# Optimization experiments

Hardware: AMD Instinct MI355X
Metric: run time of the kernel (lower is better)

## Reference

```python
import jax, jax.numpy as jnp
import numpy as np

B, C, H, W = 8, 256, 128, 128
RED = 4
LAMBDA_C = 0.5
LAMBDA_S = 0.5
EPS = 1e-5  # BatchNorm eps (eval mode: running stats)


def setup_inputs() -> dict:
    key = jax.random.key(0)
    ks = jax.random.split(key, 8)
    Cr = C // RED
    x1 = jax.random.normal(ks[0], (B, C, H, W), jnp.float32)
    x2 = jax.random.normal(ks[1], (B, C, H, W), jnp.float32)
    # feature_extractor: 1x1 conv (dim*2 -> dim), kaiming-ish scale
    w_fe = jax.random.normal(ks[2], (C, 2 * C), jnp.float32) * (2.0 / (2 * C)) ** 0.5
    bn_gamma = jnp.ones((C,), jnp.float32)
    bn_beta = jnp.zeros((C,), jnp.float32)
    bn_mean = jnp.zeros((C,), jnp.float32)
    bn_var = jnp.ones((C,), jnp.float32)
    # conv_weight_generator: C -> C//r -> 9C (1x1 convs on pooled vector)
    w_cg1 = jax.random.normal(ks[3], (Cr, C), jnp.float32) * (2.0 / C) ** 0.5
    w_cg2 = jax.random.normal(ks[4], (9 * C, Cr), jnp.float32) * (2.0 / Cr) ** 0.5
    # attention_generator: C -> C//r -> 2
    w_ag1 = jax.random.normal(ks[5], (Cr, C), jnp.float32) * (2.0 / C) ** 0.5
    w_ag2 = jax.random.normal(ks[6], (2, Cr), jnp.float32) * (2.0 / Cr) ** 0.5
    return {"x1": x1, "x2": x2, "w_fe": w_fe, "bn_gamma": bn_gamma,
            "bn_beta": bn_beta, "bn_mean": bn_mean, "bn_var": bn_var,
            "w_cg1": w_cg1, "w_cg2": w_cg2, "w_ag1": w_ag1, "w_ag2": w_ag2}


def reference(x1, x2, w_fe, bn_gamma, bn_beta, bn_mean, bn_var,
              w_cg1, w_cg2, w_ag1, w_ag2):
    Bv, Cv, Hv, Wv = x1.shape
    # feature_extractor: 1x1 conv + BN (eval) + ReLU
    cat = jnp.concatenate([x1, x2], axis=1)                       # [B,2C,H,W]
    s = jnp.einsum('oi,bihw->bohw', w_fe, cat)                    # [B,C,H,W]
    scale = (bn_gamma / jnp.sqrt(bn_var + EPS))[None, :, None, None]
    shift = (bn_beta - bn_mean * bn_gamma / jnp.sqrt(bn_var + EPS))[None, :, None, None]
    s = jax.nn.relu(s * scale + shift)
    # global average pool -> per-sample vectors
    pooled = s.mean(axis=(2, 3))                                  # [B,C]
    # dynamic per-sample, per-channel 3x3 kernels
    hcg = jax.nn.relu(pooled @ w_cg1.T)                           # [B,C//r]
    cw = (hcg @ w_cg2.T).reshape(Bv * Cv, 1, 3, 3)                # [B*C,1,3,3]
    # attention scalars (2 per sample)
    attn = jax.nn.sigmoid(jax.nn.relu(pooled @ w_ag1.T) @ w_ag2.T)  # [B,2]

    def dyn_conv(x):
        xr = x.reshape(1, Bv * Cv, Hv, Wv)
        y = jax.lax.conv_general_dilated(
            xr, cw, window_strides=(1, 1), padding='SAME',
            feature_group_count=Bv * Cv,
            dimension_numbers=('NCHW', 'OIHW', 'NCHW'))
        return y.reshape(Bv, Cv, Hv, Wv)

    d1 = dyn_conv(x1)
    d2 = dyn_conv(x2)
    a1 = attn[:, 0][:, None, None, None]
    a2 = attn[:, 1][:, None, None, None]
    out_x1 = x1 + LAMBDA_C * a1 * d1
    out_x2 = x2 + LAMBDA_C * a2 * d2
    return LAMBDA_S * out_x1 + (1.0 - LAMBDA_S) * out_x2
```

## Files before the change

### kernel.cpp

```cpp
#include <hip/hip_runtime.h>
#include <stdint.h>
#include <math.h>

#define HW_ 16384
#define C_  256
#define NT  4

typedef long i64;
typedef float f32x4 __attribute__((ext_vector_type(4)));
typedef unsigned int u32;

#define BARRIER_LGKM() asm volatile("s_waitcnt lgkmcnt(0)\n\ts_barrier" ::: "memory")

__global__ __launch_bounds__(256) void k0_prep(
    const float* __restrict__ w_fe, const float* __restrict__ gamma,
    const float* __restrict__ beta, const float* __restrict__ mean,
    const float* __restrict__ var, u32* __restrict__ Wp,
    float* __restrict__ scale, float* __restrict__ shift)
{
  int i = blockIdx.x * 256 + threadIdx.x;
  if (i < 32768) {
    int e0  = (i & 1) * 4;
    int r15 = (i >> 1) & 15;
    int kg  = (i >> 5) & 3;
    int mf  = (i >> 7) & 15;
    int ks  = i >> 11;
    int row = mf * 16 + r15;
    int k   = ks * 32 + kg * 8 + e0;
    const float* src = w_fe + row * 512 + k;
    u32 w = 0;
    w = __builtin_amdgcn_cvt_pk_fp8_f32(src[0], src[1], w, false);
    w = __builtin_amdgcn_cvt_pk_fp8_f32(src[2], src[3], w, true);
    Wp[i] = w;
  }
  if (i < 256) {
    float sc = gamma[i] * rsqrtf(var[i] + 1e-5f);
    scale[i] = sc;
    shift[i] = beta[i] - mean[i] * sc;
  }
}

__global__ __launch_bounds__(1024, 4) void k1_gemm_pool(
    const float* __restrict__ x1, const float* __restrict__ x2,
    const u32* __restrict__ Wp,
    const float* __restrict__ scale, const float* __restrict__ shift,
    float* __restrict__ pool_part)
{
  __shared__ __align__(16) char Bl[2][65536];

  const int tid  = threadIdx.x;
  const int wave = tid >> 6;
  const int lane = tid & 63;
  const int r15  = lane & 15;
  const int kg   = lane >> 4;
  const int blk  = blockIdx.x;
  const int b    = blk >> 5;
  const int j32  = blk & 31;

  const float* xb1 = x1 + (size_t)b * C_ * HW_;
  const float* xb2 = x2 + (size_t)b * C_ * HW_;

  const int o   = tid >> 5;
  const int q   = tid & 31;
  const int pq  = q * 4;
  const int wq  = (q * 32) ^ ((o & 3) << 5);

  const int rb_off = (r15 * 8) ^ (kg << 5);

  i64 Af[16];
#pragma unroll
  for (int ks = 0; ks < 16; ++ks)
    Af[ks] = *(const i64*)((const char*)Wp
             + ((ks * 16 + wave) * 64 + kg * 16 + r15) * 8);

  const int chbase = wave * 16 + kg * 4;
  const float4 sc4 = *(const float4*)&scale[chbase];
  const float4 sh4 = *(const float4*)&shift[chbase];

  float pool0 = 0.f, pool1 = 0.f, pool2 = 0.f, pool3 = 0.f;

  f32x4 gU[4];

#define ISSUE_U(H, S, P0)                                                     \
  {                                                                           \
    const float* s0 = ((H) == 0 ? xb1 : xb2)                                  \
                      + (size_t)(o * 8 + (S) * 4) * HW_ + (P0) + pq;          \
    _Pragma("unroll")                                                         \
    for (int r = 0; r < 4; ++r) gU[r] = *(const f32x4*)(s0 + r * HW_);        \
  }

#define WRITE_U(H, S, BUF)                                                    \
  {                                                                           \
    char* wb = (char*)(BUF) + ((H) * 32 + o) * 1024 + wq + (S) * 4;           \
    _Pragma("unroll")                                                         \
    for (int j = 0; j < 4; ++j) {                                             \
      u32 w = 0;                                                              \
      w = __builtin_amdgcn_cvt_pk_fp8_f32(gU[0][j], gU[1][j], w, false);      \
      w = __builtin_amdgcn_cvt_pk_fp8_f32(gU[2][j], gU[3][j], w, true);       \
      *(u32*)(wb + j * 8) = w;                                                \
    }                                                                         \
  }

#define COMPUTE_Q(QK, BUF)                                                    \
  {                                                                           \
    _Pragma("unroll")                                                         \
    for (int ks = (QK) * 4; ks < (QK) * 4 + 4; ++ks) {                        \
      const char* rb = (const char*)(BUF) + (ks * 4 + kg) * 1024 + rb_off;    \
      _Pragma("unroll")                                                       \
      for (int nf = 0; nf < 8; ++nf) {                                        \
        i64 bq = *(const i64*)(rb + nf * 128);                                \
        acc[nf] = __builtin_amdgcn_mfma_f32_16x16x32_fp8_fp8(                 \
            Af[ks], bq, acc[nf], 0, 0, 0);                                    \
      }                                                                       \
    }                                                                         \
  }

  ISSUE_U(0, 0, j32 * 128) WRITE_U(0, 0, Bl[0])
  ISSUE_U(0, 1, j32 * 128) WRITE_U(0, 1, Bl[0])
  ISSUE_U(1, 0, j32 * 128) WRITE_U(1, 0, Bl[0])
  ISSUE_U(1, 1, j32 * 128) WRITE_U(1, 1, Bl[0])
  __syncthreads();

  for (int tt = 0; tt < NT; ++tt) {
    f32x4 acc[8];
#pragma unroll
    for (int nf = 0; nf < 8; ++nf) acc[nf] = (f32x4){0.f, 0.f, 0.f, 0.f};

    const int p1 = (j32 + (tt + 1) * 32) * 128;
    const bool more = (tt + 1 < NT);
    const char* cb = Bl[tt & 1];
    char* nxt = Bl[(tt + 1) & 1];

    if (more) ISSUE_U(0, 0, p1)
    COMPUTE_Q(0, cb)
    if (more) { WRITE_U(0, 0, nxt) ISSUE_U(0, 1, p1) }
    COMPUTE_Q(1, cb)
    if (more) { WRITE_U(0, 1, nxt) ISSUE_U(1, 0, p1) }
    COMPUTE_Q(2, cb)
    if (more) { WRITE_U(1, 0, nxt) ISSUE_U(1, 1, p1) }
    COMPUTE_Q(3, cb)
    if (more) WRITE_U(1, 1, nxt)

#pragma unroll
    for (int nf = 0; nf < 8; ++nf) {
      pool0 += fmaxf(acc[nf][0] * sc4.x + sh4.x, 0.f);
      pool1 += fmaxf(acc[nf][1] * sc4.y + sh4.y, 0.f);
      pool2 += fmaxf(acc[nf][2] * sc4.z + sh4.z, 0.f);
      pool3 += fmaxf(acc[nf][3] * sc4.w + sh4.w, 0.f);
    }
    BARRIER_LGKM();
  }

#pragma unroll
  for (int m = 1; m < 16; m <<= 1) {
    pool0 += __shfl_xor(pool0, m);
    pool1 += __shfl_xor(pool1, m);
    pool2 += __shfl_xor(pool2, m);
    pool3 += __shfl_xor(pool3, m);
  }
  if (r15 == 0) {
    float* dst = pool_part + (size_t)blk * 256 + chbase;
    dst[0] = pool0; dst[1] = pool1; dst[2] = pool2; dst[3] = pool3;
  }
}

__global__ __launch_bounds__(256) void k2_small(
    const float* __restrict__ pool_part,
    const float* __restrict__ w_cg1, const float* __restrict__ w_cg2,
    const float* __restrict__ w_ag1, const float* __restrict__ w_ag2,
    float* __restrict__ cw, float* __restrict__ coef)
{
  __shared__ float pl[256];
  __shared__ float hl[64];
  const int bi = blockIdx.x;
  const int b = bi / 10, j = bi % 10;
  const int t = threadIdx.x;
  float s = 0.f;
  const float* base = pool_part + (size_t)b * 32 * 256 + t;
  for (int blk = 0; blk < 32; ++blk) s += base[blk * 256];
  pl[t] = s * (1.0f / 16384.0f);
  __syncthreads();
  if (j < 9) {
    if (t < 64) {
      float h = 0.f;
      for (int i = 0; i < 256; ++i) h += pl[i] * w_cg1[t * 256 + i];
      hl[t] = fmaxf(h, 0.f);
    }
    __syncthreads();
    const int o = t * 9 + j;
    float acc = 0.f;
    for (int jj = 0; jj < 64; ++jj) acc += hl[jj] * w_cg2[o * 64 + jj];
    cw[b * 2304 + o] = acc;
  } else {
    if (t < 64) {
      float a = 0.f;
      for (int i = 0; i < 256; ++i) a += pl[i] * w_ag1[t * 256 + i];
      hl[t] = fmaxf(a, 0.f);
    }
    __syncthreads();
    if (t < 2) {
      float acc = 0.f;
      for (int jj = 0; jj < 64; ++jj) acc += hl[jj] * w_ag2[t * 64 + jj];
      coef[b * 2 + t] = 0.25f / (1.0f + expf(-acc));
    }
  }
}

__global__ __launch_bounds__(256) void k3_dynconv(
    const float* __restrict__ x1, const float* __restrict__ x2,
    const float* __restrict__ cw, const float* __restrict__ coef,
    float* __restrict__ out)
{
  __shared__ float t1[34 * 128];
  __shared__ float t2[34 * 128];
  const int tid   = threadIdx.x;
  const int blk   = blockIdx.x;
  const int strip = blk & 3;
  const int c     = (blk >> 2) & 255;
  const int b     = blk >> 10;
  const int h0    = strip * 32;

  const size_t plane = ((size_t)b * C_ + c) * HW_;
  const float* p1 = x1 + plane;
  const float* p2 = x2 + plane;

  float tp[9];
#pragma unroll
  for (int e = 0; e < 9; ++e) tp[e] = cw[(b * C_ + c) * 9 + e];
  const float c1 = coef[b * 2 + 0];
  const float c2 = coef[b * 2 + 1];

  for (int f = tid; f < 1088; f += 256) {
    int row = f >> 5;
    int c4  = (f & 31) << 2;
    int gh  = h0 - 1 + row;
    float4 v1 = make_float4(0.f, 0.f, 0.f, 0.f), v2 = v1;
    if (gh >= 0 && gh < 128) {
      v1 = *(const float4*)&p1[gh * 128 + c4];
      v2 = *(const float4*)&p2[gh * 128 + c4];
    }
    *(float4*)&t1[row * 128 + c4] = v1;
    *(float4*)&t2[row * 128 + c4] = v2;
  }
  __syncthreads();

  for (int i = 0; i < 16; ++i) {
    int q   = tid + i * 256;
    int r   = q >> 7;
    int col = q & 127;
    int lr  = r + 1;
    const bool lok = col > 0, rok = col < 127;
    float d1 = 0.f, d2 = 0.f;
#pragma unroll
    for (int dy = 0; dy < 3; ++dy) {
      const float* row1 = &t1[(lr - 1 + dy) * 128];
      const float* row2 = &t2[(lr - 1 + dy) * 128];
      float a1v = lok ? row1[col - 1] : 0.f;
      float b1v = row1[col];
      float e1v = rok ? row1[col + 1] : 0.f;
      float a2v = lok ? row2[col - 1] : 0.f;
      float b2v = row2[col];
      float e2v = rok ? row2[col + 1] : 0.f;
      d1 += a1v * tp[dy * 3 + 0] + b1v * tp[dy * 3 + 1] + e1v * tp[dy * 3 + 2];
      d2 += a2v * tp[dy * 3 + 0] + b2v * tp[dy * 3 + 1] + e2v * tp[dy * 3 + 2];
    }
    float v1 = t1[lr * 128 + col];
    float v2 = t2[lr * 128 + col];
    out[plane + (size_t)(h0 + r) * 128 + col] = 0.5f * (v1 + v2) + c1 * d1 + c2 * d2;
  }
}

extern "C" void kernel_launch(void* const* d_in, const int* in_sizes, int n_in,
                              void* d_out, int out_size, void* d_ws, size_t ws_size,
                              hipStream_t stream) {
  const float* x1    = (const float*)d_in[0];
  const float* x2    = (const float*)d_in[1];
  const float* w_fe  = (const float*)d_in[2];
  const float* gamma = (const float*)d_in[3];
  const float* beta  = (const float*)d_in[4];
  const float* mean  = (const float*)d_in[5];
  const float* var   = (const float*)d_in[6];
  const float* w_cg1 = (const float*)d_in[7];
  const float* w_cg2 = (const float*)d_in[8];
  const float* w_ag1 = (const float*)d_in[9];
  const float* w_ag2 = (const float*)d_in[10];
  float* out = (float*)d_out;

  char* ws = (char*)d_ws;
  u32* Wp          = (u32*)(ws);
  float* scale     = (float*)(ws + 131072);
  float* shift     = (float*)(ws + 132096);
  float* pool_part = (float*)(ws + 133120);
  float* cw        = (float*)(ws + 395264);
  float* coef      = (float*)(ws + 468992);

  k0_prep<<<128, 256, 0, stream>>>(w_fe, gamma, beta, mean, var, Wp, scale, shift);
  k1_gemm_pool<<<256, 1024, 0, stream>>>(x1, x2, Wp, scale, shift, pool_part);
  k2_small<<<80, 256, 0, stream>>>(pool_part, w_cg1, w_cg2, w_ag1, w_ag2, cw, coef);
  k3_dynconv<<<8192, 256, 0, stream>>>(x1, x2, cw, coef, out);
}
```

Before: 157.7 us.

## Replace double-buffered GEMM pipeline with single large tile load-then-compute

Drops the register-staged double-buffered LDS pipeline in the fused FP8 GEMM+pool kernel. Each iteration now loads a 256-pixel tile into one 128KB LDS buffer, with 8-channel packed fp8 u64 writes and a new XOR swizzle. It then runs two compute passes over the tile, so there are half as many iterations. Overlap of global loads with MFMA work within a block is lost, and the design now relies on concurrent blocks to hide latency. The larger LDS footprint may lower occupancy.

New measurement: 243.9 us. 1.55x slower.

```diff
diff --git a/kernel.cpp b/kernel.cpp
--- a/kernel.cpp
+++ b/kernel.cpp
@@ -4,13 +4,12 @@
 
 #define HW_ 16384
 #define C_  256
-#define NT  4
+#define NT  2
 
 typedef long i64;
 typedef float f32x4 __attribute__((ext_vector_type(4)));
 typedef unsigned int u32;
-
-#define BARRIER_LGKM() asm volatile("s_waitcnt lgkmcnt(0)\n\ts_barrier" ::: "memory")
+typedef unsigned long long u64;
 
 __global__ __launch_bounds__(256) void k0_prep(
     const float* __restrict__ w_fe, const float* __restrict__ gamma,
@@ -46,7 +45,7 @@
     const float* __restrict__ scale, const float* __restrict__ shift,
     float* __restrict__ pool_part)
 {
-  __shared__ __align__(16) char Bl[2][65536];
+  __shared__ __align__(16) char Bl[131072];
 
   const int tid  = threadIdx.x;
   const int wave = tid >> 6;
@@ -55,17 +54,10 @@
   const int kg   = lane >> 4;
   const int blk  = blockIdx.x;
   const int b    = blk >> 5;
-  const int j32  = blk & 31;
+  const int jp   = blk & 31;
 
   const float* xb1 = x1 + (size_t)b * C_ * HW_;
   const float* xb2 = x2 + (size_t)b * C_ * HW_;
-
-  const int o   = tid >> 5;
-  const int q   = tid & 31;
-  const int pq  = q * 4;
-  const int wq  = (q * 32) ^ ((o & 3) << 5);
-
-  const int rb_off = (r15 * 8) ^ (kg << 5);
 
   i64 Af[16];
 #pragma unroll
@@ -79,76 +71,60 @@
 
   float pool0 = 0.f, pool1 = 0.f, pool2 = 0.f, pool3 = 0.f;
 
-  f32x4 gU[4];
-
-#define ISSUE_U(H, S, P0)                                                     \
-  {                                                                           \
-    const float* s0 = ((H) == 0 ? xb1 : xb2)                                  \
-                      + (size_t)(o * 8 + (S) * 4) * HW_ + (P0) + pq;          \
-    _Pragma("unroll")                                                         \
-    for (int r = 0; r < 4; ++r) gU[r] = *(const f32x4*)(s0 + r * HW_);        \
-  }
-
-#define WRITE_U(H, S, BUF)                                                    \
-  {                                                                           \
-    char* wb = (char*)(BUF) + ((H) * 32 + o) * 1024 + wq + (S) * 4;           \
-    _Pragma("unroll")                                                         \
-    for (int j = 0; j < 4; ++j) {                                             \
-      u32 w = 0;                                                              \
-      w = __builtin_amdgcn_cvt_pk_fp8_f32(gU[0][j], gU[1][j], w, false);      \
-      w = __builtin_amdgcn_cvt_pk_fp8_f32(gU[2][j], gU[3][j], w, true);       \
-      *(u32*)(wb + j * 8) = w;                                                \
-    }                                                                         \
-  }
-
-#define COMPUTE_Q(QK, BUF)                                                    \
-  {                                                                           \
-    _Pragma("unroll")                                                         \
-    for (int ks = (QK) * 4; ks < (QK) * 4 + 4; ++ks) {                        \
-      const char* rb = (const char*)(BUF) + (ks * 4 + kg) * 1024 + rb_off;    \
-      _Pragma("unroll")                                                       \
-      for (int nf = 0; nf < 8; ++nf) {                                        \
-        i64 bq = *(const i64*)(rb + nf * 128);                                \
-        acc[nf] = __builtin_amdgcn_mfma_f32_16x16x32_fp8_fp8(                 \
-            Af[ks], bq, acc[nf], 0, 0, 0);                                    \
-      }                                                                       \
-    }                                                                         \
-  }
-
-  ISSUE_U(0, 0, j32 * 128) WRITE_U(0, 0, Bl[0])
-  ISSUE_U(0, 1, j32 * 128) WRITE_U(0, 1, Bl[0])
-  ISSUE_U(1, 0, j32 * 128) WRITE_U(1, 0, Bl[0])
-  ISSUE_U(1, 1, j32 * 128) WRITE_U(1, 1, Bl[0])
-  __syncthreads();
-
   for (int tt = 0; tt < NT; ++tt) {
-    f32x4 acc[8];
-#pragma unroll
-    for (int nf = 0; nf < 8; ++nf) acc[nf] = (f32x4){0.f, 0.f, 0.f, 0.f};
-
-    const int p1 = (j32 + (tt + 1) * 32) * 128;
-    const bool more = (tt + 1 < NT);
-    const char* cb = Bl[tt & 1];
-    char* nxt = Bl[(tt + 1) & 1];
-
-    if (more) ISSUE_U(0, 0, p1)
-    COMPUTE_Q(0, cb)
-    if (more) { WRITE_U(0, 0, nxt) ISSUE_U(0, 1, p1) }
-    COMPUTE_Q(1, cb)
-    if (more) { WRITE_U(0, 1, nxt) ISSUE_U(1, 0, p1) }
-    COMPUTE_Q(2, cb)
-    if (more) { WRITE_U(1, 0, nxt) ISSUE_U(1, 1, p1) }
-    COMPUTE_Q(3, cb)
-    if (more) WRITE_U(1, 1, nxt)
-
-#pragma unroll
-    for (int nf = 0; nf < 8; ++nf) {
-      pool0 += fmaxf(acc[nf][0] * sc4.x + sh4.x, 0.f);
-      pool1 += fmaxf(acc[nf][1] * sc4.y + sh4.y, 0.f);
-      pool2 += fmaxf(acc[nf][2] * sc4.z + sh4.z, 0.f);
-      pool3 += fmaxf(acc[nf][3] * sc4.w + sh4.w, 0.f);
-    }
-    BARRIER_LGKM();
+    const int P0 = (jp * NT + tt) * 256;
+
+#pragma unroll
+    for (int gi = 0; gi < 4; ++gi) {
+      const int G = wave + gi * 16;
+      const float* src = ((G < 32) ? (xb1 + (size_t)(G * 8) * HW_)
+                                   : (xb2 + (size_t)(G - 32) * 8 * HW_))
+                         + P0 + lane * 4;
+      f32x4 g[8];
+#pragma unroll
+      for (int j = 0; j < 8; ++j) g[j] = *(const f32x4*)(src + (size_t)j * HW_);
+      char* rowb = Bl + G * 2048;
+#pragma unroll
+      for (int q2 = 0; q2 < 4; ++q2) {
+        u32 w0 = 0, w1 = 0;
+        w0 = __builtin_amdgcn_cvt_pk_fp8_f32(g[0][q2], g[1][q2], w0, false);
+        w0 = __builtin_amdgcn_cvt_pk_fp8_f32(g[2][q2], g[3][q2], w0, true);
+        w1 = __builtin_amdgcn_cvt_pk_fp8_f32(g[4][q2], g[5][q2], w1, false);
+        w1 = __builtin_amdgcn_cvt_pk_fp8_f32(g[6][q2], g[7][q2], w1, true);
+        int p  = lane * 4 + q2;
+        int sl = p ^ ((p >> 4) & 3) ^ ((G & 3) << 4);
+        u64 v = (u64)w0 | ((u64)w1 << 32);
+        *(u64*)(rowb + sl * 8) = v;
+      }
+    }
+    __syncthreads();
+
+#pragma unroll
+    for (int pass = 0; pass < 2; ++pass) {
+      f32x4 acc[8];
+#pragma unroll
+      for (int f = 0; f < 8; ++f) acc[f] = (f32x4){0.f, 0.f, 0.f, 0.f};
+#pragma unroll
+      for (int ks = 0; ks < 16; ++ks) {
+        const char* kb = Bl + ks * 8192 + kg * 2048;
+#pragma unroll
+        for (int f = 0; f < 8; ++f) {
+          const int nf = pass * 8 + f;
+          const int sl = (((nf ^ kg) & 15) << 4) | (r15 ^ (nf & 3));
+          i64 bq = *(const i64*)(kb + sl * 8);
+          acc[f] = __builtin_amdgcn_mfma_f32_16x16x32_fp8_fp8(
+              Af[ks], bq, acc[f], 0, 0, 0);
+        }
+      }
+#pragma unroll
+      for (int f = 0; f < 8; ++f) {
+        pool0 += fmaxf(acc[f][0] * sc4.x + sh4.x, 0.f);
+        pool1 += fmaxf(acc[f][1] * sc4.y + sh4.y, 0.f);
+        pool2 += fmaxf(acc[f][2] * sc4.z + sh4.z, 0.f);
+        pool3 += fmaxf(acc[f][3] * sc4.w + sh4.w, 0.f);
+      }
+    }
+    __syncthreads();
   }
 
 #pragma unroll
```
